# Performance work log

Hardware: AMD Instinct MI355X
Metric: run time of the kernel (lower is better)

The kernel has to match this reference:

```python
import jax, jax.numpy as jnp
import numpy as np

M, NC, NT, DX = 8, 1024, 512, 3
CHUNK = 512          # chunk_size
N_STEPS = 8          # n_steps (tol=0.0 -> torch early-stop never fires)
LR = 0.1
B1, B2, EPS = 0.9, 0.999, 1e-8
SQRT5 = 5.0 ** 0.5
LOG2PI = float(np.log(2.0 * np.pi))
NOISE_LB = 1e-4      # gpytorch GreaterThan(1e-4) noise constraint


def setup_inputs():
    key = jax.random.key(0)
    k1, k2, k3 = jax.random.split(key, 3)
    return {
        "xc": jax.random.normal(k1, (M, NC, DX), jnp.float32),
        "yc": jax.random.normal(k2, (M, NC, 1), jnp.float32),
        "xt": jax.random.normal(k3, (M, NT, DX), jnp.float32),
    }


def _kernel(x1, x2, ls, outscale):
    # ScaleKernel(MaternKernel(nu=2.5)); ls: [m,1,1], outscale: [m]
    xs1, xs2 = x1 / ls, x2 / ls
    d2 = (jnp.sum(xs1 * xs1, -1)[:, :, None]
          + jnp.sum(xs2 * xs2, -1)[:, None, :]
          - 2.0 * jnp.einsum('mnd,mkd->mnk', xs1, xs2))
    d2 = jnp.clip(d2, 1e-12, None)   # clamp like gpytorch dist for grad safety
    d = jnp.sqrt(d2)
    k = (1.0 + SQRT5 * d + (5.0 / 3.0) * d2) * jnp.exp(-SQRT5 * d)
    return outscale[:, None, None] * k


def _constrained(params):
    ls = jax.nn.softplus(params["raw_ls"])                          # [m,1,1]
    outscale = jax.nn.softplus(params["raw_os"])                    # [m]
    noise = jax.nn.softplus(params["raw_noise"][:, 0]) + NOISE_LB   # [m]
    return ls, outscale, noise


def _nll(params, x, y):
    # sum over tasks of -ExactMarginalLogLikelihood (gpytorch divides by n)
    ls, outscale, noise = _constrained(params)
    n = x.shape[1]
    K = _kernel(x, x, ls, outscale) + noise[:, None, None] * jnp.eye(n, dtype=x.dtype)
    L = jnp.linalg.cholesky(K)
    diff = y - params["const"][:, None]
    alpha = jax.scipy.linalg.cho_solve((L, True), diff[..., None])[..., 0]
    quad = jnp.sum(diff * alpha, -1)
    logdet = 2.0 * jnp.sum(jnp.log(jnp.diagonal(L, axis1=-2, axis2=-1)), -1)
    mll = -0.5 * (quad + logdet + n * LOG2PI) / n
    return jnp.sum(-mll)


def _adam_step(carry, x_sub, y_sub):
    p, m_, v_, t = carry
    g = jax.grad(_nll)(p, x_sub, y_sub)
    t = t + 1.0
    tm = jax.tree_util.tree_map
    m_ = tm(lambda a, gg: B1 * a + (1.0 - B1) * gg, m_, g)
    v_ = tm(lambda a, gg: B2 * a + (1.0 - B2) * gg * gg, v_, g)
    bc1 = 1.0 - B1 ** t
    bc2 = 1.0 - B2 ** t
    p = tm(lambda pp, mm, vv: pp - LR * (mm / bc1) / (jnp.sqrt(vv / bc2) + EPS), p, m_, v_)
    return (p, m_, v_, t)


def _gp_forward(xc, yc, xt):
    y = yc[..., 0]                                    # [m, nc]
    zl = lambda s: jnp.zeros(s, jnp.float32)
    # gpytorch raw params initialize to 0
    params = {"raw_ls": zl((M, 1, 1)), "raw_os": zl((M,)),
              "raw_noise": zl((M, 1)), "const": zl((M,))}
    m_ = jax.tree_util.tree_map(jnp.zeros_like, params)
    v_ = jax.tree_util.tree_map(jnp.zeros_like, params)
    carry = (params, m_, v_, jnp.float32(0.0))
    for i in range(0, NC, CHUNK):                     # 'Expanding' strategy
        end = min(i + CHUNK, NC)
        x_sub, y_sub = xc[:, :end], y[:, :end]
        step = lambda c, _: (_adam_step(c, x_sub, y_sub), None)
        carry, _ = jax.lax.scan(step, carry, None, length=N_STEPS)
    params = carry[0]
    # posterior predictive with trained hypers (train data = full context)
    ls, outscale, noise = _constrained(params)
    Kcc = _kernel(xc, xc, ls, outscale) + noise[:, None, None] * jnp.eye(NC, dtype=xc.dtype)
    L = jnp.linalg.cholesky(Kcc)
    diff = y - params["const"][:, None]
    alpha = jax.scipy.linalg.cho_solve((L, True), diff[..., None])[..., 0]
    Ktc = _kernel(xt, xc, ls, outscale)               # [m, nt, nc]
    mean = params["const"][:, None] + jnp.einsum('mtn,mn->mt', Ktc, alpha)
    v = jax.scipy.linalg.solve_triangular(L, jnp.swapaxes(Ktc, 1, 2), lower=True)  # [m,nc,nt]
    var_f = outscale[:, None] - jnp.sum(v * v, axis=1)  # Matern(0)=1 -> prior diag = outputscale
    var = var_f + noise[:, None]                      # likelihood(f) adds observation noise
    return jnp.stack([mean, var])                     # [2, m, nt]


def reference(xc, yc, xt):
    return _gp_forward(xc, yc, xt)
```

## Files before the change

### kernel.cpp

```cpp
#include <hip/hip_runtime.h>
#include <math.h>

constexpr int MM = 8;
constexpr int NC = 1024;
constexpr int NT = 512;
constexpr int GRID = 512;
constexpr int GPB  = GRID / MM;

constexpr size_t OFF_A     = (size_t)MM * 1024 * 1024;
constexpr size_t OFF_T     = OFF_A * 2;
constexpr size_t OFF_KTC   = OFF_T + (size_t)MM * 512 * 512;
constexpr size_t OFF_ALPHA = OFF_KTC + (size_t)MM * NT * NC;
constexpr size_t OFF_ACC   = OFF_ALPHA + (size_t)MM * 1024;

#define S5 2.2360679775f

struct GBar {
  unsigned slot[GPB][16];
  unsigned gen[16];
};
__device__ GBar g_bar2[MM];

__device__ __forceinline__ unsigned bar_base(int m) {
  return __hip_atomic_load(&g_bar2[m].gen[0], __ATOMIC_RELAXED, __HIP_MEMORY_SCOPE_AGENT);
}

__device__ __forceinline__ void gbar(int m, int gb, unsigned& ph) {
  __syncthreads();
  GBar* b = &g_bar2[m];
  const int tid = threadIdx.x;
  if (gb == 0) {
    if (tid >= 1 && tid < GPB) {
      while (__hip_atomic_load(&b->slot[tid][0], __ATOMIC_RELAXED, __HIP_MEMORY_SCOPE_AGENT) < ph)
        __builtin_amdgcn_s_sleep(2);
    }
    __syncthreads();
    if (tid == 0) {
      __threadfence();
      __hip_atomic_store(&b->gen[0], ph, __ATOMIC_RELAXED, __HIP_MEMORY_SCOPE_AGENT);
    }
    __syncthreads();
  } else {
    if (tid == 0) {
      __threadfence();
      __hip_atomic_store(&b->slot[gb][0], ph, __ATOMIC_RELAXED, __HIP_MEMORY_SCOPE_AGENT);
      while (__hip_atomic_load(&b->gen[0], __ATOMIC_RELAXED, __HIP_MEMORY_SCOPE_AGENT) < ph)
        __builtin_amdgcn_s_sleep(8);
      __threadfence();
    }
    __syncthreads();
  }
  ph++;
}

__device__ __forceinline__ float sigmf(float x) { return 1.0f / (1.0f + expf(-x)); }
__device__ __forceinline__ float softplusf(float x) { return fmaxf(x, 0.0f) + log1pf(expf(-fabsf(x))); }

__device__ __forceinline__ void lt_decode(int x, int& i, int& j) {
  int ii = 0;
  while ((ii + 1) * (ii + 2) / 2 <= x) ++ii;
  i = ii; j = x - ii * (ii + 1) / 2;
}

struct SMem {
  float Ls[64 * 65];
  float Us[64 * 65];
  float Tt[32 * 33];
  float dvec[64];
  float As[16][68];
  float Bs[16][68];
  float xi[64][3];
  float xj[64][3];
  float ai[64];
  float aj[64];
  float red[4][4];
  unsigned bar0;
};

template <int TA, int TB>
__device__ __forceinline__ void gemm64(const float* __restrict__ A, int lda,
                                       const float* __restrict__ B, int ldb,
                                       int kBeg, int kEnd, float acc[4][4], SMem& sm) {
  int tid = threadIdx.x, tx = tid & 15, ty = tid >> 4;
  float ra[4], rb[4];
  auto ldAB = [&](int k0) {
#pragma unroll
    for (int q = 0; q < 4; ++q) {
      int e = tid + (q << 8);
      if (TA) { int kk = e >> 6, r = e & 63; ra[q] = A[(size_t)(k0 + kk) * lda + r]; }
      else    { int r = e >> 4, kk = e & 15; ra[q] = A[(size_t)r * lda + k0 + kk]; }
      if (TB) { int c = e >> 4, kk = e & 15; rb[q] = B[(size_t)c * ldb + k0 + kk]; }
      else    { int kk = e >> 6, c = e & 63; rb[q] = B[(size_t)(k0 + kk) * ldb + c]; }
    }
  };
  ldAB(kBeg);
  for (int k0 = kBeg; k0 < kEnd; k0 += 16) {
    __syncthreads();
#pragma unroll
    for (int q = 0; q < 4; ++q) {
      int e = tid + (q << 8);
      if (TA) sm.As[e >> 6][e & 63] = ra[q]; else sm.As[e & 15][e >> 4] = ra[q];
      if (TB) sm.Bs[e & 15][e >> 4] = rb[q]; else sm.Bs[e >> 6][e & 63] = rb[q];
    }
    __syncthreads();
    if (k0 + 16 < kEnd) ldAB(k0 + 16);
#pragma unroll
    for (int kk = 0; kk < 16; ++kk) {
      float a[4], b[4];
#pragma unroll
      for (int i = 0; i < 4; ++i) a[i] = sm.As[kk][ty * 4 + i];
#pragma unroll
      for (int j = 0; j < 4; ++j) b[j] = sm.Bs[kk][tx * 4 + j];
#pragma unroll
      for (int i = 0; i < 4; ++i)
#pragma unroll
        for (int j = 0; j < 4; ++j) acc[i][j] = fmaf(a[i], b[j], acc[i][j]);
    }
  }
}

__device__ void factor64(SMem& sm, float* Uout, int ldu) {
  int tid = threadIdx.x;
  int tx = tid & 15, ty = tid >> 4;
  for (int j = 0; j < 63; ++j) {
    float rinv = 1.0f / sm.Ls[j * 65 + j];
    for (int i = j + 1 + ty; i < 64; i += 16) {
      float lij = sm.Ls[i * 65 + j] * rinv;
      for (int c = j + 1 + tx; c <= i; c += 16) sm.Ls[i * 65 + c] -= lij * sm.Ls[c * 65 + j];
    }
    __syncthreads();
  }
  if (tid < 64) sm.dvec[tid] = 1.0f / sqrtf(sm.Ls[tid * 65 + tid]);
  __syncthreads();
  for (int e = tid; e < 4096; e += 256) { int r = e >> 6, c = e & 63; if (c <= r) sm.Ls[r * 65 + c] *= sm.dvec[c]; }
  __syncthreads();
  for (int e = tid; e < 64 * 65; e += 256) sm.Us[e] = 0.0f;
  __syncthreads();
  if (tid < 64) {
    int b = tid >> 5, c0 = tid & 31, base = b * 32, gc = base + c0;
    sm.Us[gc * 65 + gc] = 1.0f / sm.Ls[gc * 65 + gc];
    for (int r = c0 + 1; r < 32; ++r) {
      int gr = base + r;
      float acc = 0.0f;
      for (int l = c0; l < r; ++l) acc += sm.Ls[gr * 65 + base + l] * sm.Us[(base + l) * 65 + gc];
      sm.Us[gr * 65 + gc] = -acc / sm.Ls[gr * 65 + gr];
    }
  }
  __syncthreads();
  for (int e = tid; e < 1024; e += 256) {
    int r = e >> 5, c = e & 31;
    float acc = 0.0f;
    for (int l = c; l < 32; ++l) acc += sm.Ls[(32 + r) * 65 + l] * sm.Us[l * 65 + c];
    sm.Tt[r * 33 + c] = acc;
  }
  __syncthreads();
  for (int e = tid; e < 1024; e += 256) {
    int r = e >> 5, c = e & 31;
    float acc = 0.0f;
    for (int l = 0; l <= r; ++l) acc += sm.Us[(32 + r) * 65 + 32 + l] * sm.Tt[l * 33 + c];
    sm.Us[(32 + r) * 65 + c] = -acc;
  }
  __syncthreads();
  for (int e = tid; e < 4096; e += 256) { int r = e >> 6, c = e & 63; Uout[(size_t)r * ldu + c] = sm.Us[r * 65 + c]; }
}


__device__ void adam_all(const float* __restrict__ yc, const float* __restrict__ ws,
                         int pn, int tstep, int m, int tid, SMem& sm,
                         float praw[4], float pm[4], float pv[4],
                         float& ls, float& os, float& noi, float& cm) {
  const float* al = ws + OFF_ALPHA + (size_t)m * 1024;
  const float* accp = ws + OFF_ACC + m * 8;
  const float* ym = yc + (size_t)m * NC;
  float t4 = 0, t5 = 0, t6 = 0;
  for (int i = tid; i < pn; i += 256) {
    float a = al[i];
    t4 = fmaf(a, a, t4); t5 += a; t6 = fmaf(ym[i] - cm, a, t6);
  }
  for (int off = 32; off; off >>= 1) {
    t4 += __shfl_down(t4, off); t5 += __shfl_down(t5, off); t6 += __shfl_down(t6, off);
  }
  int wid = tid >> 6, lane = tid & 63;
  if (lane == 0) { sm.red[wid][0] = t4; sm.red[wid][1] = t5; sm.red[wid][2] = t6; }
  __syncthreads();
  t4 = sm.red[0][0] + sm.red[1][0] + sm.red[2][0] + sm.red[3][0];
  t5 = sm.red[0][1] + sm.red[1][1] + sm.red[2][1] + sm.red[3][1];
  t6 = sm.red[0][2] + sm.red[1][2] + sm.red[2][2] + sm.red[3][2];
  float T1 = accp[0], T2 = accp[1], t3 = accp[2];
  float fn = (float)pn;
  float g_ls = 0.5f / fn * (T1 - T2);
  float g_os = 0.5f / (fn * os) * (fn - noi * t3 - t6 + noi * t4);
  float g_no = 0.5f / fn * (t3 - t4);
  float g_c = -t5 / fn;
  float gr[4];
  gr[0] = g_ls * sigmf(praw[0]);
  gr[1] = g_os * sigmf(praw[1]);
  gr[2] = g_no * sigmf(praw[2]);
  gr[3] = g_c;
  float bc1 = 1.0f - powf(0.9f, (float)tstep);
  float bc2 = 1.0f - powf(0.999f, (float)tstep);
#pragma unroll
  for (int i = 0; i < 4; ++i) {
    float mv = 0.9f * pm[i] + 0.1f * gr[i];
    float vv = 0.999f * pv[i] + 0.001f * gr[i] * gr[i];
    pm[i] = mv; pv[i] = vv;
    praw[i] = praw[i] - 0.1f * (mv / bc1) / (sqrtf(vv / bc2) + 1e-8f);
  }
  ls = softplusf(praw[0]);
  os = softplusf(praw[1]);
  noi = softplusf(praw[2]) + 1e-4f;
  cm = praw[3];
  __syncthreads();
}

__device__ void d_buildK(const float* __restrict__ xc, float* ws, int n, int job, int m,
                         int tid, SMem& sm, float ls, float os, float noi) {
  const float* xm = xc + (size_t)m * NC * 3;
  float* Km = ws + (size_t)m * 1048576;
  float* Am = ws + OFF_A + (size_t)m * 1048576;
  float il2 = 1.0f / (ls * ls);
  int bi, bj; lt_decode(job, bi, bj);
  if (tid < 64) {
    int r = bi * 64 + tid;
    sm.xi[tid][0] = xm[r * 3 + 0]; sm.xi[tid][1] = xm[r * 3 + 1]; sm.xi[tid][2] = xm[r * 3 + 2];
  } else if (tid < 128) {
    int lr = tid - 64; int r = bj * 64 + lr;
    sm.xj[lr][0] = xm[r * 3 + 0]; sm.xj[lr][1] = xm[r * 3 + 1]; sm.xj[lr][2] = xm[r * 3 + 2];
  }
  __syncthreads();
  if (job == 0) {
    for (int e = tid; e < 4096; e += 256) {
      int r = e >> 6, c = e & 63;
      float d0 = sm.xi[r][0] - sm.xj[c][0], d1 = sm.xi[r][1] - sm.xj[c][1], d2 = sm.xi[r][2] - sm.xj[c][2];
      float r2 = d0 * d0 + d1 * d1 + d2 * d2;
      float z = fmaxf(r2 * il2, 1e-12f);
      float dd = sqrtf(z);
      float kv = os * (1.0f + S5 * dd + (5.0f / 3.0f) * z) * expf(-S5 * dd);
      if (r == c) kv += noi;
      sm.Ls[r * 65 + c] = kv;
    }
    __syncthreads();
    factor64(sm, Am, n);
  } else {
    for (int e = tid; e < 4096; e += 256) {
      int r = e >> 6, c = e & 63;
      float d0 = sm.xi[r][0] - sm.xj[c][0], d1 = sm.xi[r][1] - sm.xj[c][1], d2 = sm.xi[r][2] - sm.xj[c][2];
      float r2 = d0 * d0 + d1 * d1 + d2 * d2;
      float z = fmaxf(r2 * il2, 1e-12f);
      float dd = sqrtf(z);
      float kv = os * (1.0f + S5 * dd + (5.0f / 3.0f) * z) * expf(-S5 * dd);
      if (bi == bj && r == c) kv += noi;
      Km[(size_t)(bi * 64 + r) * n + bj * 64 + c] = kv;
    }
  }
}

__device__ void d_trail(float* ws, int k, int n, int job, int m, int tid, SMem& sm) {
  int tx = tid & 15, ty = tid >> 4;
  float* Km = ws + (size_t)m * 1048576;
  float* Am = ws + OFF_A + (size_t)m * 1048576;
  const float* Linv = Am + (size_t)(k * 64) * n + k * 64;
  int di, dj; lt_decode(job, di, dj);
  int i = k + 1 + di, j = k + 1 + dj;
  float pp[4][4] = {};
  gemm64<0, 1>(Km + (size_t)(i * 64) * n + k * 64, n, Linv, n, 0, 64, pp, sm);
  __syncthreads();
#pragma unroll
  for (int ii = 0; ii < 4; ++ii)
#pragma unroll
    for (int jj = 0; jj < 4; ++jj) sm.Ls[(ty * 4 + ii) * 65 + tx * 4 + jj] = pp[ii][jj];
  if (di == dj) {
    float* P = Am + (size_t)(i * 64) * n + k * 64;
#pragma unroll
    for (int ii = 0; ii < 4; ++ii)
#pragma unroll
      for (int jj = 0; jj < 4; ++jj) P[(size_t)(ty * 4 + ii) * n + tx * 4 + jj] = pp[ii][jj];
  } else {
#pragma unroll
    for (int ii = 0; ii < 4; ++ii)
#pragma unroll
      for (int jj = 0; jj < 4; ++jj) pp[ii][jj] = 0.0f;
    gemm64<0, 1>(Km + (size_t)(j * 64) * n + k * 64, n, Linv, n, 0, 64, pp, sm);
#pragma unroll
    for (int ii = 0; ii < 4; ++ii)
#pragma unroll
      for (int jj = 0; jj < 4; ++jj) sm.Us[(ty * 4 + ii) * 65 + tx * 4 + jj] = pp[ii][jj];
  }
  __syncthreads();
  float acc[4][4] = {};
  {
    const float* Bsrc = (di == dj) ? sm.Ls : sm.Us;
    for (int l = 0; l < 64; ++l) {
      float a[4], b[4];
#pragma unroll
      for (int ii = 0; ii < 4; ++ii) a[ii] = sm.Ls[(ty * 4 + ii) * 65 + l];
#pragma unroll
      for (int jj = 0; jj < 4; ++jj) b[jj] = Bsrc[(tx * 4 + jj) * 65 + l];
#pragma unroll
      for (int ii = 0; ii < 4; ++ii)
#pragma unroll
        for (int jj = 0; jj < 4; ++jj) acc[ii][jj] = fmaf(a[ii], b[jj], acc[ii][jj]);
    }
  }
  float* C = Km + (size_t)(i * 64) * n + j * 64;
  if (job == 0) {
    __syncthreads();
#pragma unroll
    for (int ii = 0; ii < 4; ++ii)
#pragma unroll
      for (int jj = 0; jj < 4; ++jj)
        sm.Ls[(ty * 4 + ii) * 65 + tx * 4 + jj] =
            C[(size_t)(ty * 4 + ii) * n + tx * 4 + jj] - acc[ii][jj];
    __syncthreads();
    factor64(sm, Am + (size_t)((k + 1) * 64) * n + (k + 1) * 64, n);
  } else {
#pragma unroll
    for (int ii = 0; ii < 4; ++ii)
#pragma unroll
      for (int jj = 0; jj < 4; ++jj)
        C[(size_t)(ty * 4 + ii) * n + tx * 4 + jj] -= acc[ii][jj];
  }
}

__device__ void d_trinv64(float* ws, int n, int p, int m, int tid, SMem& sm) {
  int tx = tid & 15, ty = tid >> 4;
  float* Am = ws + OFF_A + (size_t)m * 1048576;
  int rb = (2 * p + 1) * 64, cb = 2 * p * 64;
  for (int e = tid; e < 4096; e += 256) {
    int r = e >> 6, c = e & 63;
    sm.Ls[r * 65 + c] = Am[(size_t)(rb + r) * n + cb + c];
    sm.Us[r * 65 + c] = Am[(size_t)(cb + r) * n + cb + c];
  }
  __syncthreads();
  float tt[4][4] = {};
  for (int l = 0; l < 64; ++l) {
    float a[4], b[4];
#pragma unroll
    for (int ii = 0; ii < 4; ++ii) a[ii] = sm.Ls[(ty * 4 + ii) * 65 + l];
#pragma unroll
    for (int jj = 0; jj < 4; ++jj) b[jj] = sm.Us[l * 65 + tx * 4 + jj];
#pragma unroll
    for (int ii = 0; ii < 4; ++ii)
#pragma unroll
      for (int jj = 0; jj < 4; ++jj) tt[ii][jj] = fmaf(a[ii], b[jj], tt[ii][jj]);
  }
  __syncthreads();
#pragma unroll
  for (int ii = 0; ii < 4; ++ii)
#pragma unroll
    for (int jj = 0; jj < 4; ++jj) sm.Ls[(ty * 4 + ii) * 65 + tx * 4 + jj] = tt[ii][jj];
  for (int e = tid; e < 4096; e += 256) {
    int r = e >> 6, c = e & 63;
    sm.Us[r * 65 + c] = Am[(size_t)(rb + r) * n + rb + c];
  }
  __syncthreads();
  float oo[4][4] = {};
  for (int l = 0; l < 64; ++l) {
    float a[4], b[4];
#pragma unroll
    for (int ii = 0; ii < 4; ++ii) a[ii] = sm.Us[(ty * 4 + ii) * 65 + l];
#pragma unroll
    for (int jj = 0; jj < 4; ++jj) b[jj] = sm.Ls[l * 65 + tx * 4 + jj];
#pragma unroll
    for (int ii = 0; ii < 4; ++ii)
#pragma unroll
      for (int jj = 0; jj < 4; ++jj) oo[ii][jj] = fmaf(a[ii], b[jj], oo[ii][jj]);
  }
#pragma unroll
  for (int ii = 0; ii < 4; ++ii)
#pragma unroll
    for (int jj = 0; jj < 4; ++jj)
      Am[(size_t)(rb + ty * 4 + ii) * n + cb + tx * 4 + jj] = -oo[ii][jj];
}

__device__ void d_trinvT(float* ws, int s, int n, int job, int m, int tid, SMem& sm) {
  int tx = tid & 15, ty = tid >> 4;
  float* Am = ws + OFF_A + (size_t)m * 1048576;
  float* Tm = ws + OFF_T + (size_t)m * 262144;
  int st = s >> 6;
  int p = job / (st * st), rem = job % (st * st);
  int ti = rem / st, tj = rem % st;
  int base = p * 2 * s;
  float acc[4][4] = {};
  gemm64<0, 0>(Am + (size_t)(base + s + ti * 64) * n + base, n,
               Am + (size_t)base * n + base + tj * 64, n, tj * 64, s, acc, sm);
  float* C = Tm + (size_t)p * s * s + (size_t)(ti * 64) * s + tj * 64;
#pragma unroll
  for (int ii = 0; ii < 4; ++ii)
#pragma unroll
    for (int jj = 0; jj < 4; ++jj) C[(size_t)(ty * 4 + ii) * s + tx * 4 + jj] = acc[ii][jj];
}

__device__ void d_trinvA(float* ws, int s, int n, int job, int m, int tid, SMem& sm) {
  int tx = tid & 15, ty = tid >> 4;
  float* Am = ws + OFF_A + (size_t)m * 1048576;
  const float* Tm = ws + OFF_T + (size_t)m * 262144;
  int st = s >> 6;
  int p = job / (st * st), rem = job % (st * st);
  int ti = rem / st, tj = rem % st;
  int base = p * 2 * s;
  float acc[4][4] = {};
  gemm64<0, 0>(Am + (size_t)(base + s + ti * 64) * n + base + s, n,
               Tm + (size_t)p * s * s + tj * 64, s, 0, (ti + 1) * 64, acc, sm);
  float* C = Am + (size_t)(base + s + ti * 64) * n + base + tj * 64;
#pragma unroll
  for (int ii = 0; ii < 4; ++ii)
#pragma unroll
    for (int jj = 0; jj < 4; ++jj) C[(size_t)(ty * 4 + ii) * n + tx * 4 + jj] = -acc[ii][jj];
}

__device__ void d_syrkAT(const float* __restrict__ yc, float* ws, int n, int job, int m,
                         int tid, SMem& sm, float cm) {
  int tx = tid & 15, ty = tid >> 4;
  const float* Am = ws + OFF_A + (size_t)m * 1048576;
  float* Gm = ws + (size_t)m * 1048576;
  const float* ym = yc + (size_t)m * NC;
  float* accp = ws + OFF_ACC + m * 8;
  float* al = ws + OFF_ALPHA + (size_t)m * 1024;
  int ib, jb; lt_decode(job, ib, jb);
  if (tid < 64) sm.ai[tid] = ym[ib * 64 + tid] - cm;
  else if (tid < 128) sm.aj[tid - 64] = ym[jb * 64 + tid - 64] - cm;
  float acc[4][4] = {};
  gemm64<1, 0>(Am + ib * 64, n, Am + jb * 64, n, ib * 64, n, acc, sm);
#pragma unroll
  for (int ii = 0; ii < 4; ++ii)
#pragma unroll
    for (int jj = 0; jj < 4; ++jj) {
      int r = ty * 4 + ii, c = tx * 4 + jj;
      Gm[(size_t)(ib * 64 + r) * n + jb * 64 + c] = acc[ii][jj];
      if (ib != jb) Gm[(size_t)(jb * 64 + c) * n + ib * 64 + r] = acc[ii][jj];
    }
  if (ib == jb && tx == ty) {
    atomicAdd(&accp[2], acc[0][0] + acc[1][1] + acc[2][2] + acc[3][3]);
  }
  float rowp[4];
#pragma unroll
  for (int i = 0; i < 4; ++i) {
    float s = 0.0f;
#pragma unroll
    for (int j = 0; j < 4; ++j) s = fmaf(acc[i][j], sm.aj[tx * 4 + j], s);
    rowp[i] = s;
  }
  float colp[4];
  if (ib != jb) {
#pragma unroll
    for (int j = 0; j < 4; ++j) {
      float s = 0.0f;
#pragma unroll
      for (int i = 0; i < 4; ++i) s = fmaf(acc[i][j], sm.ai[ty * 4 + i], s);
      colp[j] = s;
    }
  }
  __syncthreads();
  float* redA = &sm.As[0][0];
  float* redB = &sm.Bs[0][0];
#pragma unroll
  for (int i = 0; i < 4; ++i) redA[(ty * 4 + i) * 16 + tx] = rowp[i];
  if (ib != jb) {
#pragma unroll
    for (int j = 0; j < 4; ++j) redB[(tx * 4 + j) * 16 + ty] = colp[j];
  }
  __syncthreads();
  if (tid < 64) {
    float s = 0.0f;
#pragma unroll
    for (int q = 0; q < 16; ++q) s += redA[tid * 16 + q];
    atomicAdd(&al[ib * 64 + tid], s);
    if (ib != jb) {
      float s2 = 0.0f;
#pragma unroll
      for (int q = 0; q < 16; ++q) s2 += redB[tid * 16 + q];
      atomicAdd(&al[jb * 64 + tid], s2);
    }
  }
}

__device__ void d_reduce(const float* __restrict__ xc, float* ws, int n, int job, int m,
                         int tid, SMem& sm, float ls, float os) {
  const float* xm = xc + (size_t)m * NC * 3;
  const float* Gm = ws + (size_t)m * 1048576;
  const float* al = ws + OFF_ALPHA + (size_t)m * 1024;
  float* accp = ws + OFF_ACC + m * 8;
  float il2 = 1.0f / (ls * ls);
  float c53 = (5.0f / 3.0f) * os / ls;
  int bi, bj; lt_decode(job, bi, bj);
  float w = (bi == bj) ? 1.0f : 2.0f;
  if (tid < 64) {
    int r = bi * 64 + tid;
    sm.xi[tid][0] = xm[r * 3 + 0]; sm.xi[tid][1] = xm[r * 3 + 1]; sm.xi[tid][2] = xm[r * 3 + 2];
    sm.ai[tid] = al[r];
  } else if (tid < 128) {
    int lr = tid - 64; int r = bj * 64 + lr;
    sm.xj[lr][0] = xm[r * 3 + 0]; sm.xj[lr][1] = xm[r * 3 + 1]; sm.xj[lr][2] = xm[r * 3 + 2];
    sm.aj[lr] = al[r];
  }
  __syncthreads();
  float a1 = 0.0f, a2 = 0.0f;
  for (int e = tid; e < 4096; e += 256) {
    int r = e >> 6, c = e & 63;
    float d0 = sm.xi[r][0] - sm.xj[c][0], d1 = sm.xi[r][1] - sm.xj[c][1], d2 = sm.xi[r][2] - sm.xj[c][2];
    float r2 = d0 * d0 + d1 * d1 + d2 * d2;
    float z = fmaxf(r2 * il2, 1e-12f);
    float dd = sqrtf(z);
    float Cv = c53 * z * (1.0f + S5 * dd) * expf(-S5 * dd);
    float g = Gm[(size_t)(bi * 64 + r) * n + bj * 64 + c];
    a1 = fmaf(g, Cv, a1);
    a2 = fmaf(sm.ai[r] * sm.aj[c], Cv, a2);
  }
  a1 *= w; a2 *= w;
  for (int off = 32; off; off >>= 1) { a1 += __shfl_down(a1, off); a2 += __shfl_down(a2, off); }
  int wid = tid >> 6, lane = tid & 63;
  if (lane == 0) { sm.red[wid][0] = a1; sm.red[wid][1] = a2; }
  __syncthreads();
  if (tid == 0) {
    a1 = sm.red[0][0] + sm.red[1][0] + sm.red[2][0] + sm.red[3][0];
    a2 = sm.red[0][1] + sm.red[1][1] + sm.red[2][1] + sm.red[3][1];
    atomicAdd(&accp[0], a1);
    atomicAdd(&accp[1], a2);
  }
}

__device__ void d_buildKtc(const float* __restrict__ xt, const float* __restrict__ xc,
                           float* ws, int job, int m, int tid, SMem& sm, float ls, float os) {
  const float* xtm = xt + (size_t)m * NT * 3;
  const float* xm = xc + (size_t)m * NC * 3;
  float* Kt = ws + OFF_KTC + (size_t)m * NT * NC;
  float* Tm = ws + OFF_T + (size_t)m * 262144;
  float il2 = 1.0f / (ls * ls);
  if (job < 2) {
    int z = job * 256 + tid;
    Tm[z] = 0.0f; Tm[NT + z] = 0.0f;
  }
  int ti = job >> 4, tj = job & 15;
  if (tid < 64) {
    int r = ti * 64 + tid;
    sm.xi[tid][0] = xtm[r * 3 + 0]; sm.xi[tid][1] = xtm[r * 3 + 1]; sm.xi[tid][2] = xtm[r * 3 + 2];
  } else if (tid < 128) {
    int lr = tid - 64; int r = tj * 64 + lr;
    sm.xj[lr][0] = xm[r * 3 + 0]; sm.xj[lr][1] = xm[r * 3 + 1]; sm.xj[lr][2] = xm[r * 3 + 2];
  }
  __syncthreads();
  for (int e = tid; e < 4096; e += 256) {
    int r = e >> 6, c = e & 63;
    float d0 = sm.xi[r][0] - sm.xj[c][0], d1 = sm.xi[r][1] - sm.xj[c][1], d2 = sm.xi[r][2] - sm.xj[c][2];
    float r2 = d0 * d0 + d1 * d1 + d2 * d2;
    float z = fmaxf(r2 * il2, 1e-12f);
    float dd = sqrtf(z);
    float kv = os * (1.0f + S5 * dd + (5.0f / 3.0f) * z) * expf(-S5 * dd);
    Kt[(size_t)(ti * 64 + r) * NC + tj * 64 + c] = kv;
  }
}

__device__ void d_predW(float* ws, int job, int m, int tid, SMem& sm) {
  int tx = tid & 15, ty = tid >> 4;
  const float* Kt = ws + OFF_KTC + (size_t)m * NT * NC;
  const float* Gm = ws + (size_t)m * 1048576;
  const float* al = ws + OFF_ALPHA + (size_t)m * 1024;
  float* S1 = ws + OFF_T + (size_t)m * 262144;
  float* S2 = S1 + NT;
  int ti = job >> 4, tj = job & 15;
  if (tid < 64) sm.aj[tid] = al[tj * 64 + tid];
  float acc[4][4] = {};
  gemm64<0, 0>(Kt + (size_t)(ti * 64) * NC, NC, Gm + tj * 64, 1024, 0, 1024, acc, sm);
  float s1p[4], s2p[4];
#pragma unroll
  for (int i = 0; i < 4; ++i) {
    float a1 = 0.0f, a2 = 0.0f;
    const float* kr = Kt + (size_t)(ti * 64 + ty * 4 + i) * NC + tj * 64;
#pragma unroll
    for (int j = 0; j < 4; ++j) {
      float kv = kr[tx * 4 + j];
      a1 = fmaf(kv, sm.aj[tx * 4 + j], a1);
      a2 = fmaf(kv, acc[i][j], a2);
    }
    s1p[i] = a1; s2p[i] = a2;
  }
  __syncthreads();
  float* redA = &sm.As[0][0];
  float* redB = &sm.Bs[0][0];
#pragma unroll
  for (int i = 0; i < 4; ++i) {
    redA[(ty * 4 + i) * 16 + tx] = s1p[i];
    redB[(ty * 4 + i) * 16 + tx] = s2p[i];
  }
  __syncthreads();
  if (tid < 64) {
    float a1 = 0.0f, a2 = 0.0f;
#pragma unroll
    for (int q = 0; q < 16; ++q) { a1 += redA[tid * 16 + q]; a2 += redB[tid * 16 + q]; }
    atomicAdd(&S1[ti * 64 + tid], a1);
    atomicAdd(&S2[ti * 64 + tid], a2);
  }
}

__global__ __launch_bounds__(256, 2) void k_gp(const float* __restrict__ xc,
                                               const float* __restrict__ yc,
                                               const float* __restrict__ xt,
                                               float* ws, float* out) {
  __shared__ SMem sm;
  const int bid = blockIdx.x;
  const int m  = bid / GPB;
  const int gb = bid % GPB;
  const int tid = threadIdx.x;

  if (tid == 0) sm.bar0 = bar_base(m);
  __syncthreads();
  unsigned ph = sm.bar0 + 1;

  float praw[4] = {0.f, 0.f, 0.f, 0.f};
  float pm[4]   = {0.f, 0.f, 0.f, 0.f};
  float pv[4]   = {0.f, 0.f, 0.f, 0.f};
  float ls = 0.69314718056f, os = 0.69314718056f;
  float noi = 0.69314718056f + 1e-4f, cm = 0.0f;

  for (int step = 0; step < 17; ++step) {
    const int n = step < 8 ? 512 : 1024;
    const int nb = n >> 6;

    if (step > 0) {
      adam_all(yc, ws, step <= 8 ? 512 : 1024, step, m, tid, sm,
               praw, pm, pv, ls, os, noi, cm);
    }
    {
      const int tot = nb * (nb + 1) / 2;
      if (gb == 0) {
        __syncthreads();
        d_buildK(xc, ws, n, 0, m, tid, sm, ls, os, noi);
      } else {
        for (int q = gb; q < tot; q += GPB - 1) {
          __syncthreads();
          d_buildK(xc, ws, n, q, m, tid, sm, ls, os, noi);
        }
      }
      gbar(m, gb, ph);
    }

    for (int k = 0; k <= nb - 2; ++k) {
      const int t = nb - 1 - k;
      const int tot = t * (t + 1) / 2;
      if (gb == 0) {
        if (k == 0) {
          float* al = ws + OFF_ALPHA + (size_t)m * 1024;
          for (int z = tid; z < 1024; z += 256) al[z] = 0.0f;
          if (tid < 8) ws[OFF_ACC + m * 8 + tid] = 0.0f;
        }
        __syncthreads();
        d_trail(ws, k, n, 0, m, tid, sm);
      } else {
        for (int q = gb; q < tot; q += GPB - 1) {
          __syncthreads();
          d_trail(ws, k, n, q, m, tid, sm);
        }
      }
      gbar(m, gb, ph);
    }

    {
      const int tot = n / 128;
      for (int q = gb; q < tot; q += GPB) {
        __syncthreads();
        d_trinv64(ws, n, q, m, tid, sm);
      }
      gbar(m, gb, ph);
    }

    for (int s = 128; s < n; s <<= 1) {
      const int st = s >> 6;
      const int np = n / (2 * s);
      const int tot = np * st * st;
      for (int q = gb; q < tot; q += GPB) {
        __syncthreads();
        d_trinvT(ws, s, n, q, m, tid, sm);
      }
      gbar(m, gb, ph);
      for (int q = gb; q < tot; q += GPB) {
        __syncthreads();
        d_trinvA(ws, s, n, q, m, tid, sm);
      }
      gbar(m, gb, ph);
    }

    {
      const int tot = nb * (nb + 1) / 2;
      for (int q = gb; q < tot; q += GPB) {
        __syncthreads();
        d_syrkAT(yc, ws, n, q, m, tid, sm, cm);
      }
      gbar(m, gb, ph);
    }

    if (step < 16) {
      const int tot = nb * (nb + 1) / 2;
      for (int q = gb; q < tot; q += GPB) {
        __syncthreads();
        d_reduce(xc, ws, n, q, m, tid, sm, ls, os);
      }
      gbar(m, gb, ph);
    }
  }

  {
    for (int q = gb; q < 128; q += GPB) {
      __syncthreads();
      d_buildKtc(xt, xc, ws, q, m, tid, sm, ls, os);
    }
    gbar(m, gb, ph);
    for (int q = gb; q < 128; q += GPB) {
      __syncthreads();
      d_predW(ws, q, m, tid, sm);
    }
    gbar(m, gb, ph);
    const float* S1 = ws + OFF_T + (size_t)m * 262144;
    const float* S2 = S1 + NT;
    for (int t = gb * 256 + tid; t < NT; t += GPB * 256) {
      out[(size_t)m * NT + t] = cm + S1[t];
      out[(size_t)MM * NT + (size_t)m * NT + t] = os + noi - S2[t];
    }
  }
}

extern "C" void kernel_launch(void* const* d_in, const int* in_sizes, int n_in,
                              void* d_out, int out_size, void* d_ws, size_t ws_size,
                              hipStream_t stream) {
  const float* xc = (const float*)d_in[0];
  const float* yc = (const float*)d_in[1];
  const float* xt = (const float*)d_in[2];
  float* out = (float*)d_out;
  float* ws = (float*)d_ws;

  hipLaunchKernelGGL(k_gp, dim3(GRID), dim3(256), 0, stream, xc, yc, xt, ws, out);

  (void)in_sizes; (void)n_in; (void)out_size; (void)ws_size;
}
```

Measured before the change: 21.84 ms.

## Fuse G·C reduction into SYRK, overlap diagonal trinv with trailing updates

```diff
diff --git a/kernel.cpp b/kernel.cpp
--- a/kernel.cpp
+++ b/kernel.cpp
@@ -409,27 +409,38 @@
     for (int jj = 0; jj < 4; ++jj) C[(size_t)(ty * 4 + ii) * n + tx * 4 + jj] = -acc[ii][jj];
 }
 
-__device__ void d_syrkAT(const float* __restrict__ yc, float* ws, int n, int job, int m,
-                         int tid, SMem& sm, float cm) {
+__device__ void d_syrkAT(const float* __restrict__ yc, const float* __restrict__ xc,
+                         float* ws, int n, int job, int m, int tid, SMem& sm,
+                         float cm, float ls, float os, bool writeG) {
   int tx = tid & 15, ty = tid >> 4;
   const float* Am = ws + OFF_A + (size_t)m * 1048576;
   float* Gm = ws + (size_t)m * 1048576;
   const float* ym = yc + (size_t)m * NC;
+  const float* xm = xc + (size_t)m * NC * 3;
   float* accp = ws + OFF_ACC + m * 8;
   float* al = ws + OFF_ALPHA + (size_t)m * 1024;
   int ib, jb; lt_decode(job, ib, jb);
-  if (tid < 64) sm.ai[tid] = ym[ib * 64 + tid] - cm;
-  else if (tid < 128) sm.aj[tid - 64] = ym[jb * 64 + tid - 64] - cm;
+  if (tid < 64) {
+    int r = ib * 64 + tid;
+    sm.ai[tid] = ym[r] - cm;
+    sm.xi[tid][0] = xm[r * 3 + 0]; sm.xi[tid][1] = xm[r * 3 + 1]; sm.xi[tid][2] = xm[r * 3 + 2];
+  } else if (tid < 128) {
+    int lr = tid - 64; int r = jb * 64 + lr;
+    sm.aj[lr] = ym[r] - cm;
+    sm.xj[lr][0] = xm[r * 3 + 0]; sm.xj[lr][1] = xm[r * 3 + 1]; sm.xj[lr][2] = xm[r * 3 + 2];
+  }
   float acc[4][4] = {};
   gemm64<1, 0>(Am + ib * 64, n, Am + jb * 64, n, ib * 64, n, acc, sm);
-#pragma unroll
-  for (int ii = 0; ii < 4; ++ii)
-#pragma unroll
-    for (int jj = 0; jj < 4; ++jj) {
-      int r = ty * 4 + ii, c = tx * 4 + jj;
-      Gm[(size_t)(ib * 64 + r) * n + jb * 64 + c] = acc[ii][jj];
-      if (ib != jb) Gm[(size_t)(jb * 64 + c) * n + ib * 64 + r] = acc[ii][jj];
-    }
+  if (writeG) {
+#pragma unroll
+    for (int ii = 0; ii < 4; ++ii)
+#pragma unroll
+      for (int jj = 0; jj < 4; ++jj) {
+        int r = ty * 4 + ii, c = tx * 4 + jj;
+        Gm[(size_t)(ib * 64 + r) * n + jb * 64 + c] = acc[ii][jj];
+        if (ib != jb) Gm[(size_t)(jb * 64 + c) * n + ib * 64 + r] = acc[ii][jj];
+      }
+  }
   if (ib == jb && tx == ty) {
     atomicAdd(&accp[2], acc[0][0] + acc[1][1] + acc[2][2] + acc[3][3]);
   }
@@ -451,7 +462,30 @@
       colp[j] = s;
     }
   }
-  __syncthreads();
+  float il2 = 1.0f / (ls * ls);
+  float c53 = (5.0f / 3.0f) * os / ls;
+  float a1 = 0.0f;
+#pragma unroll
+  for (int ii = 0; ii < 4; ++ii) {
+    int r = ty * 4 + ii;
+#pragma unroll
+    for (int jj = 0; jj < 4; ++jj) {
+      int c = tx * 4 + jj;
+      float d0 = sm.xi[r][0] - sm.xj[c][0], d1 = sm.xi[r][1] - sm.xj[c][1], d2 = sm.xi[r][2] - sm.xj[c][2];
+      float r2 = d0 * d0 + d1 * d1 + d2 * d2;
+      float z = fmaxf(r2 * il2, 1e-12f);
+      float dd = sqrtf(z);
+      float Cv = c53 * z * (1.0f + S5 * dd) * expf(-S5 * dd);
+      a1 = fmaf(acc[ii][jj], Cv, a1);
+    }
+  }
+  a1 *= (ib == jb) ? 1.0f : 2.0f;
+  for (int off = 32; off; off >>= 1) a1 += __shfl_down(a1, off);
+  int wid = tid >> 6, lane = tid & 63;
+  if (lane == 0) sm.red[wid][0] = a1;
+  __syncthreads();
+  if (tid == 0)
+    atomicAdd(&accp[0], sm.red[0][0] + sm.red[1][0] + sm.red[2][0] + sm.red[3][0]);
   float* redA = &sm.As[0][0];
   float* redB = &sm.Bs[0][0];
 #pragma unroll
@@ -475,10 +509,9 @@
   }
 }
 
-__device__ void d_reduce(const float* __restrict__ xc, float* ws, int n, int job, int m,
-                         int tid, SMem& sm, float ls, float os) {
+__device__ void d_reduce2(const float* __restrict__ xc, float* ws, int n, int job, int m,
+                          int tid, SMem& sm, float ls, float os) {
   const float* xm = xc + (size_t)m * NC * 3;
-  const float* Gm = ws + (size_t)m * 1048576;
   const float* al = ws + OFF_ALPHA + (size_t)m * 1024;
   float* accp = ws + OFF_ACC + m * 8;
   float il2 = 1.0f / (ls * ls);
@@ -495,7 +528,7 @@
     sm.aj[lr] = al[r];
   }
   __syncthreads();
-  float a1 = 0.0f, a2 = 0.0f;
+  float a2 = 0.0f;
   for (int e = tid; e < 4096; e += 256) {
     int r = e >> 6, c = e & 63;
     float d0 = sm.xi[r][0] - sm.xj[c][0], d1 = sm.xi[r][1] - sm.xj[c][1], d2 = sm.xi[r][2] - sm.xj[c][2];
@@ -503,20 +536,15 @@
     float z = fmaxf(r2 * il2, 1e-12f);
     float dd = sqrtf(z);
     float Cv = c53 * z * (1.0f + S5 * dd) * expf(-S5 * dd);
-    float g = Gm[(size_t)(bi * 64 + r) * n + bj * 64 + c];
-    a1 = fmaf(g, Cv, a1);
     a2 = fmaf(sm.ai[r] * sm.aj[c], Cv, a2);
   }
-  a1 *= w; a2 *= w;
-  for (int off = 32; off; off >>= 1) { a1 += __shfl_down(a1, off); a2 += __shfl_down(a2, off); }
+  a2 *= w;
+  for (int off = 32; off; off >>= 1) a2 += __shfl_down(a2, off);
   int wid = tid >> 6, lane = tid & 63;
-  if (lane == 0) { sm.red[wid][0] = a1; sm.red[wid][1] = a2; }
+  if (lane == 0) sm.red[wid][1] = a2;
   __syncthreads();
   if (tid == 0) {
-    a1 = sm.red[0][0] + sm.red[1][0] + sm.red[2][0] + sm.red[3][0];
-    a2 = sm.red[0][1] + sm.red[1][1] + sm.red[2][1] + sm.red[3][1];
-    atomicAdd(&accp[0], a1);
-    atomicAdd(&accp[1], a2);
+    atomicAdd(&accp[1], sm.red[0][1] + sm.red[1][1] + sm.red[2][1] + sm.red[3][1]);
   }
 }
 
@@ -599,8 +627,8 @@
                                                float* ws, float* out) {
   __shared__ SMem sm;
   const int bid = blockIdx.x;
-  const int m  = bid / GPB;
-  const int gb = bid % GPB;
+  const int m  = bid % MM;
+  const int gb = bid / MM;
   const int tid = threadIdx.x;
 
   if (tid == 0) sm.bar0 = bar_base(m);
@@ -616,6 +644,7 @@
   for (int step = 0; step < 17; ++step) {
     const int n = step < 8 ? 512 : 1024;
     const int nb = n >> 6;
+    const bool lastStep = (step == 16);
 
     if (step > 0) {
       adam_all(yc, ws, step <= 8 ? 512 : 1024, step, m, tid, sm,
@@ -651,15 +680,10 @@
           __syncthreads();
           d_trail(ws, k, n, q, m, tid, sm);
         }
-      }
-      gbar(m, gb, ph);
-    }
-
-    {
-      const int tot = n / 128;
-      for (int q = gb; q < tot; q += GPB) {
-        __syncthreads();
-        d_trinv64(ws, n, q, m, tid, sm);
+        if ((k & 1) && gb == GPB - 1) {
+          __syncthreads();
+          d_trinv64(ws, n, k >> 1, m, tid, sm);
+        }
       }
       gbar(m, gb, ph);
     }
@@ -672,6 +696,10 @@
         __syncthreads();
         d_trinvT(ws, s, n, q, m, tid, sm);
       }
+      if (s == 128 && gb == GPB - 1) {
+        __syncthreads();
+        d_trinv64(ws, n, nb / 2 - 1, m, tid, sm);
+      }
       gbar(m, gb, ph);
       for (int q = gb; q < tot; q += GPB) {
         __syncthreads();
@@ -684,7 +712,7 @@
       const int tot = nb * (nb + 1) / 2;
       for (int q = gb; q < tot; q += GPB) {
         __syncthreads();
-        d_syrkAT(yc, ws, n, q, m, tid, sm, cm);
+        d_syrkAT(yc, xc, ws, n, q, m, tid, sm, cm, ls, os, lastStep);
       }
       gbar(m, gb, ph);
     }
@@ -693,7 +721,7 @@
       const int tot = nb * (nb + 1) / 2;
       for (int q = gb; q < tot; q += GPB) {
         __syncthreads();
-        d_reduce(xc, ws, n, q, m, tid, sm, ls, os);
+        d_reduce2(xc, ws, n, q, m, tid, sm, ls, os);
       }
       gbar(m, gb, ph);
     }
```

After: 22.36 ms. 2.3% more time.
